# Kernel optimization log

Measured on AMD Instinct MI355X. Metric: run time of the kernel, lower is better.

Reference implementation:

```python
import jax, jax.numpy as jnp
import numpy as np

EMBED = 1024
B, I, J = 8, 2048, 2048
SCALE = EMBED ** -0.5


def setup_inputs() -> dict:
    key = jax.random.key(0)
    ks = jax.random.split(key, 5)
    s = EMBED ** -0.5  # init scale for weights
    return {
        "q_in": jax.random.normal(ks[0], (B, I, EMBED), dtype=jnp.float32),
        "k_v": jax.random.normal(ks[1], (B, J, EMBED), dtype=jnp.float32),
        "Wq": jax.random.normal(ks[2], (EMBED, EMBED), dtype=jnp.float32) * s,
        "bq": jnp.zeros((EMBED,), dtype=jnp.float32),
        "Wk": jax.random.normal(ks[3], (EMBED, EMBED), dtype=jnp.float32) * s,
        "bk": jnp.zeros((EMBED,), dtype=jnp.float32),
        "Wv": jax.random.normal(ks[4], (EMBED, EMBED), dtype=jnp.float32) * s,
        "bv": jnp.zeros((EMBED,), dtype=jnp.float32),
    }


def reference(q_in, k_v, Wq, bq, Wk, bk, Wv, bv):
    # Linear projections (torch Linear: x @ W.T + b; here W stored as [in, out])
    q = q_in @ Wq + bq            # [b, i, d]
    k = k_v @ Wk + bk             # [b, j, d]
    v = k_v @ Wv + bv             # [b, j, d]
    sim = jnp.einsum('bid,bjd->bij', q, k) * SCALE  # [b, i, j]
    attn = jax.nn.softmax(sim, axis=-1)
    # dropout with drop_rate=0.0 is identity
    out = jnp.einsum('bij,bjd->bid', attn, v)       # [b, i, d]
    return out
```

## Files before the change

kernel.cpp:

```cpp
#include <hip/hip_runtime.h>
#include <hip/hip_bf16.h>


#define BATCH 8
#define SEQ   2048
#define EMB   1024
#define SC2   0.045084222f

typedef __attribute__((ext_vector_type(8))) short bf16x8;
typedef __attribute__((ext_vector_type(4))) float f32x4;
typedef __attribute__((ext_vector_type(4))) unsigned short u16x4;
typedef __attribute__((ext_vector_type(8))) unsigned short u16x8;
typedef __attribute__((ext_vector_type(4))) float fl4;

__device__ __forceinline__ unsigned short f2bf(float f) {
    unsigned u = __builtin_bit_cast(unsigned, f);
    unsigned r = u + 0x7fffu + ((u >> 16) & 1u);
    return (unsigned short)(r >> 16);
}
__device__ __forceinline__ float bf2f(unsigned short s) {
    return __builtin_bit_cast(float, ((unsigned)s) << 16);
}
__device__ __forceinline__ void gload16(const unsigned short* g, unsigned short* l) {
    __builtin_amdgcn_global_load_lds(
        (const __attribute__((address_space(1))) void*)g,
        (__attribute__((address_space(3))) void*)l, 16, 0, 0);
}

__global__ __launch_bounds__(256)
void convert_in(const float* __restrict__ q_in, const float* __restrict__ k_v,
                unsigned short* __restrict__ qbin, unsigned short* __restrict__ kvbin)
{
    const size_t N = (size_t)BATCH * SEQ * EMB;
    size_t idx = ((size_t)blockIdx.x * 256 + threadIdx.x) * 8;
    const size_t stride = (size_t)gridDim.x * 256 * 8;
    for (; idx < N; idx += stride) {
        fl4 a0 = *(const fl4*)&q_in[idx];
        fl4 a1 = *(const fl4*)&q_in[idx + 4];
        fl4 b0 = *(const fl4*)&k_v[idx];
        fl4 b1 = *(const fl4*)&k_v[idx + 4];
        u16x8 ua, ub;
#pragma unroll
        for (int i = 0; i < 4; i++) {
            ua[i] = f2bf(a0[i]); ua[i + 4] = f2bf(a1[i]);
            ub[i] = f2bf(b0[i]); ub[i + 4] = f2bf(b1[i]);
        }
        *(u16x8*)&qbin[idx] = ua;
        *(u16x8*)&kvbin[idx] = ub;
    }
}

__global__ __launch_bounds__(256)
void convert_w(const float* __restrict__ Wq, const float* __restrict__ Wk,
               const float* __restrict__ Wv, unsigned short* __restrict__ Wt)
{
    const int wsel = blockIdx.y;
    const float* W = (wsel == 0) ? Wq : (wsel == 1) ? Wk : Wv;
    unsigned short* O = Wt + (size_t)wsel * EMB * EMB;
    const int k0 = (blockIdx.x >> 4) * 64;
    const int n0 = (blockIdx.x & 15) * 64;
    __shared__ unsigned short l[64 * 65];
    const int tid = threadIdx.x;
#pragma unroll
    for (int it = 0; it < 16; it++) {
        const int lin = it * 256 + tid;
        const int k = lin >> 6, n = lin & 63;
        l[n * 65 + k] = f2bf(W[(size_t)(k0 + k) * EMB + n0 + n]);
    }
    __syncthreads();
#pragma unroll
    for (int it = 0; it < 16; it++) {
        const int lin = it * 256 + tid;
        const int n = lin >> 6, k = lin & 63;
        O[(size_t)(n0 + n) * EMB + k0 + k] = l[n * 65 + k];
    }
}

__device__ __forceinline__ void stageT(const unsigned short* lanebase, size_t rstride,
                                       unsigned short* lwave) {
#pragma unroll
    for (int i = 0; i < 2; i++)
        gload16(lanebase + (size_t)(i * 128) * rstride, lwave + i * 4096);
}

#define PIPE_PHASE1(SLOT, DO_STAGE, STAGE_A_BASE, STAGE_A_LDS)                  \
    {                                                                           \
        const unsigned short* pa = &sA[SLOT][0];                                \
        const unsigned short* pb = &sB[SLOT][0];                                \
        bf16x8 a0 = *(bf16x8*)&pa[aoff0];                                       \
        bf16x8 a1 = *(bf16x8*)&pa[aoff0 + 512];                                 \
        bf16x8 a2 = *(bf16x8*)&pa[aoff0 + 1024];                                \
        bf16x8 a3 = *(bf16x8*)&pa[aoff0 + 1536];                                \
        bv0 = *(bf16x8*)&pb[boff0];                                             \
        bv1 = *(bf16x8*)&pb[boff0 + 512];                                       \
        bv2 = *(bf16x8*)&pb[boff0 + 1024];                                      \
        bv3 = *(bf16x8*)&pb[boff0 + 1536];                                      \
        if (DO_STAGE) stageT(STAGE_A_BASE, strideA, STAGE_A_LDS);               \
        __builtin_amdgcn_s_barrier();                                           \
        asm volatile("s_waitcnt lgkmcnt(0)" ::: "memory");                      \
        __builtin_amdgcn_sched_barrier(0);                                      \
        __builtin_amdgcn_s_setprio(1);                                          \
        acc[0][0] = __builtin_amdgcn_mfma_f32_16x16x32_bf16(a0, bv0, acc[0][0], 0, 0, 0); \
        acc[0][1] = __builtin_amdgcn_mfma_f32_16x16x32_bf16(a0, bv1, acc[0][1], 0, 0, 0); \
        acc[0][2] = __builtin_amdgcn_mfma_f32_16x16x32_bf16(a0, bv2, acc[0][2], 0, 0, 0); \
        acc[0][3] = __builtin_amdgcn_mfma_f32_16x16x32_bf16(a0, bv3, acc[0][3], 0, 0, 0); \
        acc[1][0] = __builtin_amdgcn_mfma_f32_16x16x32_bf16(a1, bv0, acc[1][0], 0, 0, 0); \
        acc[1][1] = __builtin_amdgcn_mfma_f32_16x16x32_bf16(a1, bv1, acc[1][1], 0, 0, 0); \
        acc[1][2] = __builtin_amdgcn_mfma_f32_16x16x32_bf16(a1, bv2, acc[1][2], 0, 0, 0); \
        acc[1][3] = __builtin_amdgcn_mfma_f32_16x16x32_bf16(a1, bv3, acc[1][3], 0, 0, 0); \
        acc[2][0] = __builtin_amdgcn_mfma_f32_16x16x32_bf16(a2, bv0, acc[2][0], 0, 0, 0); \
        acc[2][1] = __builtin_amdgcn_mfma_f32_16x16x32_bf16(a2, bv1, acc[2][1], 0, 0, 0); \
        acc[2][2] = __builtin_amdgcn_mfma_f32_16x16x32_bf16(a2, bv2, acc[2][2], 0, 0, 0); \
        acc[2][3] = __builtin_amdgcn_mfma_f32_16x16x32_bf16(a2, bv3, acc[2][3], 0, 0, 0); \
        acc[3][0] = __builtin_amdgcn_mfma_f32_16x16x32_bf16(a3, bv0, acc[3][0], 0, 0, 0); \
        acc[3][1] = __builtin_amdgcn_mfma_f32_16x16x32_bf16(a3, bv1, acc[3][1], 0, 0, 0); \
        acc[3][2] = __builtin_amdgcn_mfma_f32_16x16x32_bf16(a3, bv2, acc[3][2], 0, 0, 0); \
        acc[3][3] = __builtin_amdgcn_mfma_f32_16x16x32_bf16(a3, bv3, acc[3][3], 0, 0, 0); \
        __builtin_amdgcn_s_setprio(0);                                          \
        __builtin_amdgcn_s_barrier();                                           \
        __builtin_amdgcn_sched_barrier(0);                                      \
    }

#define PIPE_PHASE2(SLOT, DO_STAGE, STAGE_B_BASE, STAGE_B_LDS)                  \
    {                                                                           \
        const unsigned short* pa = &sA[SLOT][0];                                \
        bf16x8 a0 = *(bf16x8*)&pa[aoff0 + 2048];                                \
        bf16x8 a1 = *(bf16x8*)&pa[aoff0 + 2560];                                \
        bf16x8 a2 = *(bf16x8*)&pa[aoff0 + 3072];                                \
        bf16x8 a3 = *(bf16x8*)&pa[aoff0 + 3584];                                \
        if (DO_STAGE) stageT(STAGE_B_BASE, strideB, STAGE_B_LDS);               \
        __builtin_amdgcn_s_barrier();                                           \
        asm volatile("s_waitcnt lgkmcnt(0)" ::: "memory");                      \
        __builtin_amdgcn_sched_barrier(0);                                      \
        __builtin_amdgcn_s_setprio(1);                                          \
        acc[4][0] = __builtin_amdgcn_mfma_f32_16x16x32_bf16(a0, bv0, acc[4][0], 0, 0, 0); \
        acc[4][1] = __builtin_amdgcn_mfma_f32_16x16x32_bf16(a0, bv1, acc[4][1], 0, 0, 0); \
        acc[4][2] = __builtin_amdgcn_mfma_f32_16x16x32_bf16(a0, bv2, acc[4][2], 0, 0, 0); \
        acc[4][3] = __builtin_amdgcn_mfma_f32_16x16x32_bf16(a0, bv3, acc[4][3], 0, 0, 0); \
        acc[5][0] = __builtin_amdgcn_mfma_f32_16x16x32_bf16(a1, bv0, acc[5][0], 0, 0, 0); \
        acc[5][1] = __builtin_amdgcn_mfma_f32_16x16x32_bf16(a1, bv1, acc[5][1], 0, 0, 0); \
        acc[5][2] = __builtin_amdgcn_mfma_f32_16x16x32_bf16(a1, bv2, acc[5][2], 0, 0, 0); \
        acc[5][3] = __builtin_amdgcn_mfma_f32_16x16x32_bf16(a1, bv3, acc[5][3], 0, 0, 0); \
        acc[6][0] = __builtin_amdgcn_mfma_f32_16x16x32_bf16(a2, bv0, acc[6][0], 0, 0, 0); \
        acc[6][1] = __builtin_amdgcn_mfma_f32_16x16x32_bf16(a2, bv1, acc[6][1], 0, 0, 0); \
        acc[6][2] = __builtin_amdgcn_mfma_f32_16x16x32_bf16(a2, bv2, acc[6][2], 0, 0, 0); \
        acc[6][3] = __builtin_amdgcn_mfma_f32_16x16x32_bf16(a2, bv3, acc[6][3], 0, 0, 0); \
        acc[7][0] = __builtin_amdgcn_mfma_f32_16x16x32_bf16(a3, bv0, acc[7][0], 0, 0, 0); \
        acc[7][1] = __builtin_amdgcn_mfma_f32_16x16x32_bf16(a3, bv1, acc[7][1], 0, 0, 0); \
        acc[7][2] = __builtin_amdgcn_mfma_f32_16x16x32_bf16(a3, bv2, acc[7][2], 0, 0, 0); \
        acc[7][3] = __builtin_amdgcn_mfma_f32_16x16x32_bf16(a3, bv3, acc[7][3], 0, 0, 0); \
        __builtin_amdgcn_s_setprio(0);                                          \
        asm volatile("s_waitcnt vmcnt(4)" ::: "memory");                        \
        __builtin_amdgcn_s_barrier();                                           \
        __builtin_amdgcn_sched_barrier(0);                                      \
    }

__device__ __forceinline__ void pipe_gemm(
    const unsigned short* __restrict__ Asrc,
    const unsigned short* __restrict__ Bsrc,
    const size_t strideA, const size_t strideB, const int NT,
    unsigned short (*sA)[8192], unsigned short (*sB)[8192],
    const int lwave, const int aoff0, const int boff0,
    f32x4 acc[8][4])
{
    stageT(Asrc, strideA, &sA[0][lwave]);
    stageT(Bsrc, strideB, &sB[0][lwave]);
    stageT(Asrc + 32, strideA, &sA[1][lwave]);
    stageT(Bsrc + 32, strideB, &sB[1][lwave]);
    asm volatile("s_waitcnt vmcnt(4)" ::: "memory");
    __builtin_amdgcn_s_barrier();
    __builtin_amdgcn_sched_barrier(0);

    bf16x8 bv0, bv1, bv2, bv3;
    for (int T = 0; T < NT; ++T) {
        const int s = T & 3;
        const int doStage = (T + 2 < NT);
        const int s2 = (T + 2) & 3;
        PIPE_PHASE1(s, doStage, Asrc + (T + 2) * 32, &sA[s2][lwave]);
        PIPE_PHASE2(s, doStage, Bsrc + (T + 2) * 32, &sB[s2][lwave]);
    }
}

#define PIPE_PREAMBLE                                                     \
    __shared__ unsigned short sMem[65536];                    \
    unsigned short (*sA)[8192] = (unsigned short (*)[8192])sMem;          \
    unsigned short (*sB)[8192] = (unsigned short (*)[8192])(sMem + 32768);\
    const int tid = threadIdx.x, lane = tid & 63;                         \
    const int wid = tid >> 6, wr = wid >> 2, wn = wid & 3;                \
    const int r = lane & 15, g = lane >> 4;                               \
    const int lwave = (wid << 9);                                         \
    const int aoff0 = (wr * 128 + r) * 32 + g * 8;                        \
    const int boff0 = (wn * 64 + r) * 32 + g * 8;                         \
    f32x4 acc[8][4];                                                      \
    _Pragma("unroll") for (int i_ = 0; i_ < 8; i_++)                      \
    _Pragma("unroll") for (int j_ = 0; j_ < 4; j_++) acc[i_][j_] = (f32x4)0.0f;

__device__ __forceinline__ void lds_flush_bf16(const unsigned short* sP,
                                               unsigned short* gbase,
                                               size_t gstride, int tid)
{
    const int lane = tid & 63, wv = tid >> 6;
    const int rowsel = lane >> 5, jj = lane & 31;
#pragma unroll
    for (int it = 0; it < 16; ++it) {
        const int row = it * 16 + wv * 2 + rowsel;
        const int byte = row * 512 + ((jj * 16) ^ ((row & 7) << 4));
        u16x8 v = *(const u16x8*)((const char*)sP + byte);
        *(u16x8*)&gbase[(size_t)row * gstride + jj * 8] = v;
    }
}

__global__ __launch_bounds__(512, 1)
void proj_q256(const unsigned short* __restrict__ Wqt,
               const unsigned short* __restrict__ X,
               const float* __restrict__ bias,
               unsigned short* __restrict__ qb)
{
    PIPE_PREAMBLE
    const int bid = blockIdx.x;
    const int lid = (bid & 7) * 32 + (bid >> 3);
    const int dt = lid & 3, it = lid >> 2;
    const int d0 = dt * 256, i0 = it * 256;
    const size_t strideA = EMB, strideB = EMB;
    const unsigned short* Asrc = Wqt + (size_t)(d0 + (tid >> 2)) * EMB + (tid & 3) * 8;
    const unsigned short* Bsrc = X + (size_t)(i0 + (tid >> 2)) * EMB + (tid & 3) * 8;

    pipe_gemm(Asrc, Bsrc, strideA, strideB, EMB / 32, sA, sB, lwave, aoff0, boff0, acc);

#pragma unroll
    for (int mm = 0; mm < 8; mm++) {
        const int colb = wr * 128 + mm * 16 + g * 4;
        const fl4 b4 = *(const fl4*)&bias[d0 + colb];
#pragma unroll
        for (int n = 0; n < 4; n++) {
            const int row = wn * 64 + n * 16 + r;
            u16x4 u;
#pragma unroll
            for (int c = 0; c < 4; c++) u[c] = f2bf(acc[mm][n][c] + b4[c]);
            const int byte = row * 512 + ((colb * 2) ^ ((row & 7) << 4));
            *(u16x4*)((char*)sMem + byte) = u;
        }
    }
    __syncthreads();
    lds_flush_bf16(sMem, qb + (size_t)i0 * EMB + d0, EMB, tid);
}

__global__ __launch_bounds__(512, 1)
void proj_kv256(const unsigned short* __restrict__ X,
                const unsigned short* __restrict__ Wkvt,
                const float* __restrict__ bk, const float* __restrict__ bv,
                unsigned short* __restrict__ kb, unsigned short* __restrict__ vt)
{
    PIPE_PREAMBLE
    const int bid = blockIdx.x;
    const int lid = (bid & 7) * 64 + (bid >> 3);
    const int nt = lid & 7, mt = lid >> 3;
    const int m0 = mt * 256, n0 = nt * 256;
    const size_t strideA = EMB, strideB = EMB;
    const unsigned short* Asrc = X + (size_t)(m0 + (tid >> 2)) * EMB + (tid & 3) * 8;
    const unsigned short* Bsrc = Wkvt + (size_t)(n0 + (tid >> 2)) * EMB + (tid & 3) * 8;

    pipe_gemm(Asrc, Bsrc, strideA, strideB, EMB / 32, sA, sB, lwave, aoff0, boff0, acc);

    const int b = m0 >> 11;
    const int j0l = m0 & 2047;
    if (n0 < 1024) {
#pragma unroll
        for (int mm = 0; mm < 8; mm++) {
            const int ibase = m0 + wr * 128 + mm * 16 + g * 4;
#pragma unroll
            for (int n = 0; n < 4; n++) {
                const int col = n0 + wn * 64 + n * 16 + r;
                const float bb = bk[col];
#pragma unroll
                for (int c = 0; c < 4; c++)
                    kb[(size_t)(ibase + c) * EMB + col] = f2bf(acc[mm][n][c] + bb);
            }
        }
    } else {
#pragma unroll
        for (int mm = 0; mm < 8; mm++) {
            const int colb = wr * 128 + mm * 16 + g * 4;
#pragma unroll
            for (int n = 0; n < 4; n++) {
                const int row = wn * 64 + n * 16 + r;
                const float bb = bv[n0 - 1024 + row];
                u16x4 u;
#pragma unroll
                for (int c = 0; c < 4; c++) u[c] = f2bf(acc[mm][n][c] + bb);
                const int byte = row * 512 + ((colb * 2) ^ ((row & 7) << 4));
                *(u16x4*)((char*)sMem + byte) = u;
            }
        }
        __syncthreads();
        lds_flush_bf16(sMem, vt + ((size_t)b * EMB + (n0 - 1024)) * SEQ + j0l,
                       SEQ, tid);
    }
}

__global__ __launch_bounds__(512, 1)
void qk256_kernel(const unsigned short* __restrict__ qb,
                  const unsigned short* __restrict__ kb,
                  unsigned short* __restrict__ P,
                  float* __restrict__ Ppart)
{
    PIPE_PREAMBLE
    const int bid = blockIdx.x;
    const int lid = (bid & 7) * 64 + (bid >> 3);
    const int b = lid >> 6, jt = (lid >> 3) & 7, it = lid & 7;
    const int j0 = jt * 256, i0 = it * 256;
    const size_t strideA = EMB, strideB = EMB;
    const unsigned short* Ag = kb + (size_t)b * SEQ * EMB;
    const unsigned short* Bg = qb + (size_t)b * SEQ * EMB;
    const unsigned short* Asrc = Ag + (size_t)(j0 + (tid >> 2)) * EMB + (tid & 3) * 8;
    const unsigned short* Bsrc = Bg + (size_t)(i0 + (tid >> 2)) * EMB + (tid & 3) * 8;

    pipe_gemm(Asrc, Bsrc, strideA, strideB, EMB / 32, sA, sB, lwave, aoff0, boff0, acc);

    float ps[4] = {0.f, 0.f, 0.f, 0.f};
#pragma unroll
    for (int mm = 0; mm < 8; mm++) {
        const int colb = wr * 128 + mm * 16 + g * 4;
#pragma unroll
        for (int n = 0; n < 4; n++) {
            const int row = wn * 64 + n * 16 + r;
            u16x4 u;
#pragma unroll
            for (int c = 0; c < 4; c++) {
                const float p = exp2f(acc[mm][n][c] * SC2);
                ps[n] += p;
                u[c] = f2bf(p);
            }
            const int byte = row * 512 + ((colb * 2) ^ ((row & 7) << 4));
            *(u16x4*)((char*)sMem + byte) = u;
        }
    }
#pragma unroll
    for (int n = 0; n < 4; n++) {
        ps[n] += __shfl_xor(ps[n], 16);
        ps[n] += __shfl_xor(ps[n], 32);
    }
    if (g == 0) {
        const int slot = jt * 2 + wr;
        float* pp = Ppart + (size_t)slot * (BATCH * SEQ) + (size_t)b * SEQ;
#pragma unroll
        for (int n = 0; n < 4; n++)
            pp[i0 + wn * 64 + n * 16 + r] = ps[n];
    }
    __syncthreads();
    unsigned short* Pb = P + (size_t)b * SEQ * SEQ;
    lds_flush_bf16(sMem, Pb + (size_t)i0 * SEQ + j0, SEQ, tid);
}

__global__ __launch_bounds__(256)
void rowsum_final(const float* __restrict__ Ppart, float* __restrict__ rs)
{
    const int row = blockIdx.x * 256 + threadIdx.x;
    float s = 0.f;
#pragma unroll
    for (int slot = 0; slot < 16; slot++)
        s += Ppart[(size_t)slot * (BATCH * SEQ) + row];
    rs[row] = s;
}

__global__ __launch_bounds__(512, 1)
void pv256_kernel(const unsigned short* __restrict__ P,
                  const unsigned short* __restrict__ vt,
                  const float* __restrict__ rs,
                  float* __restrict__ out)
{
    PIPE_PREAMBLE
    const int bid = blockIdx.x;
    const int lid = (bid & 7) * 32 + (bid >> 3);
    const int b = lid >> 5, it = (lid >> 2) & 7, dt = lid & 3;
    const int d0 = dt * 256, i0 = it * 256;
    const size_t strideA = SEQ, strideB = SEQ;
    const unsigned short* Ag = vt + (size_t)b * EMB * SEQ;
    const unsigned short* Bg = P + (size_t)b * SEQ * SEQ;
    const unsigned short* Asrc = Ag + (size_t)(d0 + (tid >> 2)) * SEQ + (tid & 3) * 8;
    const unsigned short* Bsrc = Bg + (size_t)(i0 + (tid >> 2)) * SEQ + (tid & 3) * 8;

    pipe_gemm(Asrc, Bsrc, strideA, strideB, SEQ / 32, sA, sB, lwave, aoff0, boff0, acc);

    float* ob = out + (size_t)b * SEQ * EMB;
    const float* rsb = rs + (size_t)b * SEQ;
    float inv[4];
#pragma unroll
    for (int n = 0; n < 4; n++)
        inv[n] = 1.0f / rsb[i0 + wn * 64 + n * 16 + r];

    float* sF = (float*)sMem;
#pragma unroll
    for (int h = 0; h < 2; h++) {
        if (wr == h) {
#pragma unroll
            for (int mm = 0; mm < 8; mm++) {
                const int colb = mm * 16 + g * 4;
#pragma unroll
                for (int n = 0; n < 4; n++) {
                    const int row = wn * 64 + n * 16 + r;
                    fl4 o;
#pragma unroll
                    for (int c = 0; c < 4; c++) o[c] = acc[mm][n][c] * inv[n];
                    const int byte = row * 512 + ((colb * 4) ^ ((row & 7) << 4));
                    *(fl4*)((char*)sF + byte) = o;
                }
            }
        }
        __syncthreads();
        {
            const int rowsel = lane >> 5, jj = lane & 31;
#pragma unroll
            for (int itx = 0; itx < 16; ++itx) {
                const int row = itx * 16 + wid * 2 + rowsel;
                const int byte = row * 512 + ((jj * 16) ^ ((row & 7) << 4));
                fl4 v = *(const fl4*)((const char*)sF + byte);
                *(fl4*)&ob[(size_t)(i0 + row) * EMB + d0 + h * 128 + jj * 4] = v;
            }
        }
        if (h == 0) __syncthreads();
    }
}

extern "C" void kernel_launch(void* const* d_in, const int* in_sizes, int n_in,
                              void* d_out, int out_size, void* d_ws, size_t ws_size,
                              hipStream_t stream)
{
    const float* q_in = (const float*)d_in[0];
    const float* k_v  = (const float*)d_in[1];
    const float* Wq   = (const float*)d_in[2];
    const float* bq   = (const float*)d_in[3];
    const float* Wk   = (const float*)d_in[4];
    const float* bk   = (const float*)d_in[5];
    const float* Wv   = (const float*)d_in[6];
    const float* bv   = (const float*)d_in[7];
    float* out = (float*)d_out;

    char* ws = (char*)d_ws;
    unsigned short* qbin = (unsigned short*)(ws);
    unsigned short* kvbin= (unsigned short*)(ws + (size_t)33554432);
    unsigned short* P    = (unsigned short*)(ws);
    unsigned short* qb   = (unsigned short*)(ws + (size_t)67108864);
    unsigned short* kb   = (unsigned short*)(ws + (size_t)100663296);
    unsigned short* vt   = (unsigned short*)(ws + (size_t)134217728);
    unsigned short* Wt   = (unsigned short*)(ws + (size_t)167772160);
    float*          Ppart= (float*)(ws + (size_t)174063616);
    float*          rs   = (float*)(ws + (size_t)175112192);

    convert_in<<<4096, 256, 0, stream>>>(q_in, k_v, qbin, kvbin);
    convert_w<<<dim3(256, 3), 256, 0, stream>>>(Wq, Wk, Wv, Wt);
    proj_q256<<<256, 512, 0, stream>>>(Wt, qbin, bq, qb);
    proj_kv256<<<512, 512, 0, stream>>>(kvbin, Wt + (size_t)EMB * EMB, bk, bv, kb, vt);
    qk256_kernel<<<512, 512, 0, stream>>>(qb, kb, P, Ppart);
    rowsum_final<<<64, 256, 0, stream>>>(Ppart, rs);
    pv256_kernel<<<256, 512, 0, stream>>>(P, vt, rs, out);
}
```

Before: 315.2 us.

## Merge launches and collapse the GEMM pipeline into one barrier phase per tile

Folds the input and weight conversion kernels into one launch, and the Q and KV projections into one 768-block launch. The row-sum reduction kernel is removed and its work is done inside the PV kernel before its GEMM. Separately, the pipelined GEMM's two barrier-separated half-tile phases are merged into one tile step, which drops one barrier pair per K-step but keeps all eight A fragments live at once. This cuts launch gaps and tail effects, at the risk of higher register pressure and a different wait pattern in the inner loop.

```diff
diff --git a/kernel.cpp b/kernel.cpp
--- a/kernel.cpp
+++ b/kernel.cpp
@@ -28,51 +28,53 @@
 }
 
 __global__ __launch_bounds__(256)
-void convert_in(const float* __restrict__ q_in, const float* __restrict__ k_v,
-                unsigned short* __restrict__ qbin, unsigned short* __restrict__ kvbin)
-{
-    const size_t N = (size_t)BATCH * SEQ * EMB;
-    size_t idx = ((size_t)blockIdx.x * 256 + threadIdx.x) * 8;
-    const size_t stride = (size_t)gridDim.x * 256 * 8;
-    for (; idx < N; idx += stride) {
-        fl4 a0 = *(const fl4*)&q_in[idx];
-        fl4 a1 = *(const fl4*)&q_in[idx + 4];
-        fl4 b0 = *(const fl4*)&k_v[idx];
-        fl4 b1 = *(const fl4*)&k_v[idx + 4];
-        u16x8 ua, ub;
-#pragma unroll
-        for (int i = 0; i < 4; i++) {
-            ua[i] = f2bf(a0[i]); ua[i + 4] = f2bf(a1[i]);
-            ub[i] = f2bf(b0[i]); ub[i + 4] = f2bf(b1[i]);
-        }
-        *(u16x8*)&qbin[idx] = ua;
-        *(u16x8*)&kvbin[idx] = ub;
-    }
-}
-
-__global__ __launch_bounds__(256)
-void convert_w(const float* __restrict__ Wq, const float* __restrict__ Wk,
-               const float* __restrict__ Wv, unsigned short* __restrict__ Wt)
-{
-    const int wsel = blockIdx.y;
-    const float* W = (wsel == 0) ? Wq : (wsel == 1) ? Wk : Wv;
-    unsigned short* O = Wt + (size_t)wsel * EMB * EMB;
-    const int k0 = (blockIdx.x >> 4) * 64;
-    const int n0 = (blockIdx.x & 15) * 64;
-    __shared__ unsigned short l[64 * 65];
+void convert_all(const float* __restrict__ q_in, const float* __restrict__ k_v,
+                 const float* __restrict__ Wq, const float* __restrict__ Wk,
+                 const float* __restrict__ Wv,
+                 unsigned short* __restrict__ qbin, unsigned short* __restrict__ kvbin,
+                 unsigned short* __restrict__ Wt)
+{
+    const int bid = blockIdx.x;
     const int tid = threadIdx.x;
-#pragma unroll
-    for (int it = 0; it < 16; it++) {
-        const int lin = it * 256 + tid;
-        const int k = lin >> 6, n = lin & 63;
-        l[n * 65 + k] = f2bf(W[(size_t)(k0 + k) * EMB + n0 + n]);
-    }
-    __syncthreads();
-#pragma unroll
-    for (int it = 0; it < 16; it++) {
-        const int lin = it * 256 + tid;
-        const int n = lin >> 6, k = lin & 63;
-        O[(size_t)(n0 + n) * EMB + k0 + k] = l[n * 65 + k];
+    if (bid < 4096) {
+        const size_t N = (size_t)BATCH * SEQ * EMB;
+        size_t idx = ((size_t)bid * 256 + tid) * 8;
+        const size_t stride = (size_t)4096 * 256 * 8;
+        for (; idx < N; idx += stride) {
+            fl4 a0 = *(const fl4*)&q_in[idx];
+            fl4 a1 = *(const fl4*)&q_in[idx + 4];
+            fl4 b0 = *(const fl4*)&k_v[idx];
+            fl4 b1 = *(const fl4*)&k_v[idx + 4];
+            u16x8 ua, ub;
+#pragma unroll
+            for (int i = 0; i < 4; i++) {
+                ua[i] = f2bf(a0[i]); ua[i + 4] = f2bf(a1[i]);
+                ub[i] = f2bf(b0[i]); ub[i + 4] = f2bf(b1[i]);
+            }
+            *(u16x8*)&qbin[idx] = ua;
+            *(u16x8*)&kvbin[idx] = ub;
+        }
+    } else {
+        const int b2 = bid - 4096;
+        const int wsel = b2 >> 8, rest = b2 & 255;
+        const float* W = (wsel == 0) ? Wq : (wsel == 1) ? Wk : Wv;
+        unsigned short* O = Wt + (size_t)wsel * EMB * EMB;
+        const int k0 = (rest >> 4) * 64;
+        const int n0 = (rest & 15) * 64;
+        __shared__ unsigned short l[64 * 65];
+#pragma unroll
+        for (int it = 0; it < 16; it++) {
+            const int lin = it * 256 + tid;
+            const int k = lin >> 6, n = lin & 63;
+            l[n * 65 + k] = f2bf(W[(size_t)(k0 + k) * EMB + n0 + n]);
+        }
+        __syncthreads();
+#pragma unroll
+        for (int it = 0; it < 16; it++) {
+            const int lin = it * 256 + tid;
+            const int n = lin >> 6, k = lin & 63;
+            O[(size_t)(n0 + n) * EMB + k0 + k] = l[n * 65 + k];
+        }
     }
 }
 
@@ -83,7 +85,7 @@
         gload16(lanebase + (size_t)(i * 128) * rstride, lwave + i * 4096);
 }
 
-#define PIPE_PHASE1(SLOT, DO_STAGE, STAGE_A_BASE, STAGE_A_LDS)                  \
+#define PIPE_TILE(SLOT, DO_STAGE, STAGE_A_BASE, STAGE_A_LDS, STAGE_B_BASE, STAGE_B_LDS) \
     {                                                                           \
         const unsigned short* pa = &sA[SLOT][0];                                \
         const unsigned short* pb = &sB[SLOT][0];                                \
@@ -91,10 +93,14 @@
         bf16x8 a1 = *(bf16x8*)&pa[aoff0 + 512];                                 \
         bf16x8 a2 = *(bf16x8*)&pa[aoff0 + 1024];                                \
         bf16x8 a3 = *(bf16x8*)&pa[aoff0 + 1536];                                \
-        bv0 = *(bf16x8*)&pb[boff0];                                             \
-        bv1 = *(bf16x8*)&pb[boff0 + 512];                                       \
-        bv2 = *(bf16x8*)&pb[boff0 + 1024];                                      \
-        bv3 = *(bf16x8*)&pb[boff0 + 1536];                                      \
+        bf16x8 a4 = *(bf16x8*)&pa[aoff0 + 2048];                                \
+        bf16x8 a5 = *(bf16x8*)&pa[aoff0 + 2560];                                \
+        bf16x8 a6 = *(bf16x8*)&pa[aoff0 + 3072];                                \
+        bf16x8 a7 = *(bf16x8*)&pa[aoff0 + 3584];                                \
+        bf16x8 bv0 = *(bf16x8*)&pb[boff0];                                      \
+        bf16x8 bv1 = *(bf16x8*)&pb[boff0 + 512];                                \
+        bf16x8 bv2 = *(bf16x8*)&pb[boff0 + 1024];                               \
+        bf16x8 bv3 = *(bf16x8*)&pb[boff0 + 1536];                               \
         if (DO_STAGE) stageT(STAGE_A_BASE, strideA, STAGE_A_LDS);               \
         __builtin_amdgcn_s_barrier();                                           \
         asm volatile("s_waitcnt lgkmcnt(0)" ::: "memory");                      \
@@ -117,38 +123,24 @@
         acc[3][2] = __builtin_amdgcn_mfma_f32_16x16x32_bf16(a3, bv2, acc[3][2], 0, 0, 0); \
         acc[3][3] = __builtin_amdgcn_mfma_f32_16x16x32_bf16(a3, bv3, acc[3][3], 0, 0, 0); \
         __builtin_amdgcn_s_setprio(0);                                          \
-        __builtin_amdgcn_s_barrier();                                           \
-        __builtin_amdgcn_sched_barrier(0);                                      \
-    }
-
-#define PIPE_PHASE2(SLOT, DO_STAGE, STAGE_B_BASE, STAGE_B_LDS)                  \
-    {                                                                           \
-        const unsigned short* pa = &sA[SLOT][0];                                \
-        bf16x8 a0 = *(bf16x8*)&pa[aoff0 + 2048];                                \
-        bf16x8 a1 = *(bf16x8*)&pa[aoff0 + 2560];                                \
-        bf16x8 a2 = *(bf16x8*)&pa[aoff0 + 3072];                                \
-        bf16x8 a3 = *(bf16x8*)&pa[aoff0 + 3584];                                \
         if (DO_STAGE) stageT(STAGE_B_BASE, strideB, STAGE_B_LDS);               \
-        __builtin_amdgcn_s_barrier();                                           \
-        asm volatile("s_waitcnt lgkmcnt(0)" ::: "memory");                      \
-        __builtin_amdgcn_sched_barrier(0);                                      \
         __builtin_amdgcn_s_setprio(1);                                          \
-        acc[4][0] = __builtin_amdgcn_mfma_f32_16x16x32_bf16(a0, bv0, acc[4][0], 0, 0, 0); \
-        acc[4][1] = __builtin_amdgcn_mfma_f32_16x16x32_bf16(a0, bv1, acc[4][1], 0, 0, 0); \
-        acc[4][2] = __builtin_amdgcn_mfma_f32_16x16x32_bf16(a0, bv2, acc[4][2], 0, 0, 0); \
-        acc[4][3] = __builtin_amdgcn_mfma_f32_16x16x32_bf16(a0, bv3, acc[4][3], 0, 0, 0); \
-        acc[5][0] = __builtin_amdgcn_mfma_f32_16x16x32_bf16(a1, bv0, acc[5][0], 0, 0, 0); \
-        acc[5][1] = __builtin_amdgcn_mfma_f32_16x16x32_bf16(a1, bv1, acc[5][1], 0, 0, 0); \
-        acc[5][2] = __builtin_amdgcn_mfma_f32_16x16x32_bf16(a1, bv2, acc[5][2], 0, 0, 0); \
-        acc[5][3] = __builtin_amdgcn_mfma_f32_16x16x32_bf16(a1, bv3, acc[5][3], 0, 0, 0); \
-        acc[6][0] = __builtin_amdgcn_mfma_f32_16x16x32_bf16(a2, bv0, acc[6][0], 0, 0, 0); \
-        acc[6][1] = __builtin_amdgcn_mfma_f32_16x16x32_bf16(a2, bv1, acc[6][1], 0, 0, 0); \
-        acc[6][2] = __builtin_amdgcn_mfma_f32_16x16x32_bf16(a2, bv2, acc[6][2], 0, 0, 0); \
-        acc[6][3] = __builtin_amdgcn_mfma_f32_16x16x32_bf16(a2, bv3, acc[6][3], 0, 0, 0); \
-        acc[7][0] = __builtin_amdgcn_mfma_f32_16x16x32_bf16(a3, bv0, acc[7][0], 0, 0, 0); \
-        acc[7][1] = __builtin_amdgcn_mfma_f32_16x16x32_bf16(a3, bv1, acc[7][1], 0, 0, 0); \
-        acc[7][2] = __builtin_amdgcn_mfma_f32_16x16x32_bf16(a3, bv2, acc[7][2], 0, 0, 0); \
-        acc[7][3] = __builtin_amdgcn_mfma_f32_16x16x32_bf16(a3, bv3, acc[7][3], 0, 0, 0); \
+        acc[4][0] = __builtin_amdgcn_mfma_f32_16x16x32_bf16(a4, bv0, acc[4][0], 0, 0, 0); \
+        acc[4][1] = __builtin_amdgcn_mfma_f32_16x16x32_bf16(a4, bv1, acc[4][1], 0, 0, 0); \
+        acc[4][2] = __builtin_amdgcn_mfma_f32_16x16x32_bf16(a4, bv2, acc[4][2], 0, 0, 0); \
+        acc[4][3] = __builtin_amdgcn_mfma_f32_16x16x32_bf16(a4, bv3, acc[4][3], 0, 0, 0); \
+        acc[5][0] = __builtin_amdgcn_mfma_f32_16x16x32_bf16(a5, bv0, acc[5][0], 0, 0, 0); \
+        acc[5][1] = __builtin_amdgcn_mfma_f32_16x16x32_bf16(a5, bv1, acc[5][1], 0, 0, 0); \
+        acc[5][2] = __builtin_amdgcn_mfma_f32_16x16x32_bf16(a5, bv2, acc[5][2], 0, 0, 0); \
+        acc[5][3] = __builtin_amdgcn_mfma_f32_16x16x32_bf16(a5, bv3, acc[5][3], 0, 0, 0); \
+        acc[6][0] = __builtin_amdgcn_mfma_f32_16x16x32_bf16(a6, bv0, acc[6][0], 0, 0, 0); \
+        acc[6][1] = __builtin_amdgcn_mfma_f32_16x16x32_bf16(a6, bv1, acc[6][1], 0, 0, 0); \
+        acc[6][2] = __builtin_amdgcn_mfma_f32_16x16x32_bf16(a6, bv2, acc[6][2], 0, 0, 0); \
+        acc[6][3] = __builtin_amdgcn_mfma_f32_16x16x32_bf16(a6, bv3, acc[6][3], 0, 0, 0); \
+        acc[7][0] = __builtin_amdgcn_mfma_f32_16x16x32_bf16(a7, bv0, acc[7][0], 0, 0, 0); \
+        acc[7][1] = __builtin_amdgcn_mfma_f32_16x16x32_bf16(a7, bv1, acc[7][1], 0, 0, 0); \
+        acc[7][2] = __builtin_amdgcn_mfma_f32_16x16x32_bf16(a7, bv2, acc[7][2], 0, 0, 0); \
+        acc[7][3] = __builtin_amdgcn_mfma_f32_16x16x32_bf16(a7, bv3, acc[7][3], 0, 0, 0); \
         __builtin_amdgcn_s_setprio(0);                                          \
         asm volatile("s_waitcnt vmcnt(4)" ::: "memory");                        \
         __builtin_amdgcn_s_barrier();                                           \
@@ -171,13 +163,12 @@
     __builtin_amdgcn_s_barrier();
     __builtin_amdgcn_sched_barrier(0);
 
-    bf16x8 bv0, bv1, bv2, bv3;
     for (int T = 0; T < NT; ++T) {
         const int s = T & 3;
         const int doStage = (T + 2 < NT);
         const int s2 = (T + 2) & 3;
-        PIPE_PHASE1(s, doStage, Asrc + (T + 2) * 32, &sA[s2][lwave]);
-        PIPE_PHASE2(s, doStage, Bsrc + (T + 2) * 32, &sB[s2][lwave]);
+        PIPE_TILE(s, doStage, Asrc + (T + 2) * 32, &sA[s2][lwave],
+                  Bsrc + (T + 2) * 32, &sB[s2][lwave]);
     }
 }
 
@@ -211,90 +202,88 @@
 }
 
 __global__ __launch_bounds__(512, 1)
-void proj_q256(const unsigned short* __restrict__ Wqt,
-               const unsigned short* __restrict__ X,
-               const float* __restrict__ bias,
-               unsigned short* __restrict__ qb)
+void proj_all(const unsigned short* __restrict__ Wt,
+              const unsigned short* __restrict__ qbin,
+              const unsigned short* __restrict__ kvbin,
+              const float* __restrict__ bq, const float* __restrict__ bk,
+              const float* __restrict__ bv,
+              unsigned short* __restrict__ qb, unsigned short* __restrict__ kb,
+              unsigned short* __restrict__ vt)
 {
     PIPE_PREAMBLE
     const int bid = blockIdx.x;
-    const int lid = (bid & 7) * 32 + (bid >> 3);
-    const int dt = lid & 3, it = lid >> 2;
-    const int d0 = dt * 256, i0 = it * 256;
     const size_t strideA = EMB, strideB = EMB;
-    const unsigned short* Asrc = Wqt + (size_t)(d0 + (tid >> 2)) * EMB + (tid & 3) * 8;
-    const unsigned short* Bsrc = X + (size_t)(i0 + (tid >> 2)) * EMB + (tid & 3) * 8;
+    const unsigned short* Asrc;
+    const unsigned short* Bsrc;
+    int d0 = 0, i0 = 0, m0 = 0, n0 = 0;
+    const bool qrole = (bid < 256);
+    if (qrole) {
+        const int lid = (bid & 7) * 32 + (bid >> 3);
+        d0 = (lid & 3) * 256; i0 = (lid >> 2) * 256;
+        Asrc = Wt + (size_t)(d0 + (tid >> 2)) * EMB + (tid & 3) * 8;
+        Bsrc = qbin + (size_t)(i0 + (tid >> 2)) * EMB + (tid & 3) * 8;
+    } else {
+        const int b2 = bid - 256;
+        const int lid = (b2 & 7) * 64 + (b2 >> 3);
+        n0 = (lid & 7) * 256; m0 = (lid >> 3) * 256;
+        Asrc = kvbin + (size_t)(m0 + (tid >> 2)) * EMB + (tid & 3) * 8;
+        Bsrc = Wt + (size_t)EMB * EMB + (size_t)(n0 + (tid >> 2)) * EMB + (tid & 3) * 8;
+    }
 
     pipe_gemm(Asrc, Bsrc, strideA, strideB, EMB / 32, sA, sB, lwave, aoff0, boff0, acc);
 
-#pragma unroll
-    for (int mm = 0; mm < 8; mm++) {
-        const int colb = wr * 128 + mm * 16 + g * 4;
-        const fl4 b4 = *(const fl4*)&bias[d0 + colb];
-#pragma unroll
-        for (int n = 0; n < 4; n++) {
-            const int row = wn * 64 + n * 16 + r;
-            u16x4 u;
-#pragma unroll
-            for (int c = 0; c < 4; c++) u[c] = f2bf(acc[mm][n][c] + b4[c]);
-            const int byte = row * 512 + ((colb * 2) ^ ((row & 7) << 4));
-            *(u16x4*)((char*)sMem + byte) = u;
-        }
-    }
-    __syncthreads();
-    lds_flush_bf16(sMem, qb + (size_t)i0 * EMB + d0, EMB, tid);
-}
-
-__global__ __launch_bounds__(512, 1)
-void proj_kv256(const unsigned short* __restrict__ X,
-                const unsigned short* __restrict__ Wkvt,
-                const float* __restrict__ bk, const float* __restrict__ bv,
-                unsigned short* __restrict__ kb, unsigned short* __restrict__ vt)
-{
-    PIPE_PREAMBLE
-    const int bid = blockIdx.x;
-    const int lid = (bid & 7) * 64 + (bid >> 3);
-    const int nt = lid & 7, mt = lid >> 3;
-    const int m0 = mt * 256, n0 = nt * 256;
-    const size_t strideA = EMB, strideB = EMB;
-    const unsigned short* Asrc = X + (size_t)(m0 + (tid >> 2)) * EMB + (tid & 3) * 8;
-    const unsigned short* Bsrc = Wkvt + (size_t)(n0 + (tid >> 2)) * EMB + (tid & 3) * 8;
-
-    pipe_gemm(Asrc, Bsrc, strideA, strideB, EMB / 32, sA, sB, lwave, aoff0, boff0, acc);
-
-    const int b = m0 >> 11;
-    const int j0l = m0 & 2047;
-    if (n0 < 1024) {
-#pragma unroll
-        for (int mm = 0; mm < 8; mm++) {
-            const int ibase = m0 + wr * 128 + mm * 16 + g * 4;
-#pragma unroll
-            for (int n = 0; n < 4; n++) {
-                const int col = n0 + wn * 64 + n * 16 + r;
-                const float bb = bk[col];
-#pragma unroll
-                for (int c = 0; c < 4; c++)
-                    kb[(size_t)(ibase + c) * EMB + col] = f2bf(acc[mm][n][c] + bb);
-            }
-        }
-    } else {
+    if (qrole) {
 #pragma unroll
         for (int mm = 0; mm < 8; mm++) {
             const int colb = wr * 128 + mm * 16 + g * 4;
+            const fl4 b4 = *(const fl4*)&bq[d0 + colb];
 #pragma unroll
             for (int n = 0; n < 4; n++) {
                 const int row = wn * 64 + n * 16 + r;
-                const float bb = bv[n0 - 1024 + row];
                 u16x4 u;
 #pragma unroll
-                for (int c = 0; c < 4; c++) u[c] = f2bf(acc[mm][n][c] + bb);
+                for (int c = 0; c < 4; c++) u[c] = f2bf(acc[mm][n][c] + b4[c]);
                 const int byte = row * 512 + ((colb * 2) ^ ((row & 7) << 4));
                 *(u16x4*)((char*)sMem + byte) = u;
             }
         }
         __syncthreads();
-        lds_flush_bf16(sMem, vt + ((size_t)b * EMB + (n0 - 1024)) * SEQ + j0l,
-                       SEQ, tid);
+        lds_flush_bf16(sMem, qb + (size_t)i0 * EMB + d0, EMB, tid);
+    } else {
+        const int b = m0 >> 11;
+        const int j0l = m0 & 2047;
+        if (n0 < 1024) {
+#pragma unroll
+            for (int mm = 0; mm < 8; mm++) {
+                const int ibase = m0 + wr * 128 + mm * 16 + g * 4;
+#pragma unroll
+                for (int n = 0; n < 4; n++) {
+                    const int col = n0 + wn * 64 + n * 16 + r;
+                    const float bb = bk[col];
+#pragma unroll
+                    for (int c = 0; c < 4; c++)
+                        kb[(size_t)(ibase + c) * EMB + col] = f2bf(acc[mm][n][c] + bb);
+                }
+            }
+        } else {
+#pragma unroll
+            for (int mm = 0; mm < 8; mm++) {
+                const int colb = wr * 128 + mm * 16 + g * 4;
+#pragma unroll
+                for (int n = 0; n < 4; n++) {
+                    const int row = wn * 64 + n * 16 + r;
+                    const float bb = bv[n0 - 1024 + row];
+                    u16x4 u;
+#pragma unroll
+                    for (int c = 0; c < 4; c++) u[c] = f2bf(acc[mm][n][c] + bb);
+                    const int byte = row * 512 + ((colb * 2) ^ ((row & 7) << 4));
+                    *(u16x4*)((char*)sMem + byte) = u;
+                }
+            }
+            __syncthreads();
+            lds_flush_bf16(sMem, vt + ((size_t)b * EMB + (n0 - 1024)) * SEQ + j0l,
+                           SEQ, tid);
+        }
     }
 }
 
@@ -352,21 +341,10 @@
     lds_flush_bf16(sMem, Pb + (size_t)i0 * SEQ + j0, SEQ, tid);
 }
 
-__global__ __launch_bounds__(256)
-void rowsum_final(const float* __restrict__ Ppart, float* __restrict__ rs)
-{
-    const int row = blockIdx.x * 256 + threadIdx.x;
-    float s = 0.f;
-#pragma unroll
-    for (int slot = 0; slot < 16; slot++)
-        s += Ppart[(size_t)slot * (BATCH * SEQ) + row];
-    rs[row] = s;
-}
-
 __global__ __launch_bounds__(512, 1)
 void pv256_kernel(const unsigned short* __restrict__ P,
                   const unsigned short* __restrict__ vt,
-                  const float* __restrict__ rs,
+                  const float* __restrict__ Ppart,
                   float* __restrict__ out)
 {
     PIPE_PREAMBLE
@@ -380,15 +358,20 @@
     const unsigned short* Asrc = Ag + (size_t)(d0 + (tid >> 2)) * SEQ + (tid & 3) * 8;
     const unsigned short* Bsrc = Bg + (size_t)(i0 + (tid >> 2)) * SEQ + (tid & 3) * 8;
 
+    float inv[4];
+#pragma unroll
+    for (int n = 0; n < 4; n++) {
+        const int row = (size_t)0 + b * SEQ + i0 + wn * 64 + n * 16 + r;
+        float s = 0.f;
+#pragma unroll
+        for (int slot = 0; slot < 16; slot++)
+            s += Ppart[(size_t)slot * (BATCH * SEQ) + row];
+        inv[n] = 1.0f / s;
+    }
+
     pipe_gemm(Asrc, Bsrc, strideA, strideB, SEQ / 32, sA, sB, lwave, aoff0, boff0, acc);
 
     float* ob = out + (size_t)b * SEQ * EMB;
-    const float* rsb = rs + (size_t)b * SEQ;
-    float inv[4];
-#pragma unroll
-    for (int n = 0; n < 4; n++)
-        inv[n] = 1.0f / rsb[i0 + wn * 64 + n * 16 + r];
-
     float* sF = (float*)sMem;
 #pragma unroll
     for (int h = 0; h < 2; h++) {
@@ -445,13 +428,9 @@
     unsigned short* vt   = (unsigned short*)(ws + (size_t)134217728);
     unsigned short* Wt   = (unsigned short*)(ws + (size_t)167772160);
     float*          Ppart= (float*)(ws + (size_t)174063616);
-    float*          rs   = (float*)(ws + (size_t)175112192);
-
-    convert_in<<<4096, 256, 0, stream>>>(q_in, k_v, qbin, kvbin);
-    convert_w<<<dim3(256, 3), 256, 0, stream>>>(Wq, Wk, Wv, Wt);
-    proj_q256<<<256, 512, 0, stream>>>(Wt, qbin, bq, qb);
-    proj_kv256<<<512, 512, 0, stream>>>(kvbin, Wt + (size_t)EMB * EMB, bk, bv, kb, vt);
+
+    convert_all<<<4864, 256, 0, stream>>>(q_in, k_v, Wq, Wk, Wv, qbin, kvbin, Wt);
+    proj_all<<<768, 512, 0, stream>>>(Wt, qbin, kvbin, bq, bk, bv, qb, kb, vt);
     qk256_kernel<<<512, 512, 0, stream>>>(qb, kb, P, Ppart);
-    rowsum_final<<<64, 256, 0, stream>>>(Ppart, rs);
-    pv256_kernel<<<256, 512, 0, stream>>>(P, vt, rs, out);
-}
+    pv256_kernel<<<256, 512, 0, stream>>>(P, vt, Ppart, out);
+}
```

Measured after the change: 311.5 us. About the same (-1.1%).
